# Kernel optimization log

Measured on AMD Instinct MI355X. Metric: run time of the kernel, lower is better.

## Reference

```python
import jax, jax.numpy as jnp
import numpy as np

N_NODES = 500000
FEAT_DIM = 128
BATCH = 50000
K = 16


def setup_inputs() -> dict:
    key = jax.random.key(0)
    k1, k2, k3 = jax.random.split(key, 3)
    features = jax.random.normal(k1, (N_NODES, FEAT_DIM), dtype=jnp.float32)
    # weights = pow(degree, beta); positive floats (uniform in (0.05, 1.05))
    neigh_w = jax.random.uniform(k2, (BATCH, K), dtype=jnp.float32) + 0.05
    neigh_idx = jax.random.randint(k3, (BATCH, K), 0, N_NODES, dtype=jnp.int64)
    return {"features": features, "neigh_w": neigh_w, "neigh_idx": neigh_idx}


def reference(features, neigh_w, neigh_idx):
    # Row-normalize weights (mask = mask.div(mask.sum(1, keepdim=True)))
    w = neigh_w / jnp.sum(neigh_w, axis=-1, keepdims=True)  # [B, K]
    # Gather neighbor embeddings (features(unique_nodes) + sparse mask rows)
    gathered = features[neigh_idx]  # [B, K, D]
    # mask.mm(embed_matrix) == weighted mean over sampled neighbors
    to_feats = jnp.einsum("bk,bkd->bd", w, gathered)  # [B, D]
    return to_feats
```

## Files before the change

### kernel.cpp

```cpp
#include <hip/hip_runtime.h>

#define KNEIGH 16
#define FDIM   128

typedef float f32x4 __attribute__((ext_vector_type(4)));

__global__ __launch_bounds__(256) void WeightedAggregator_89489938580183_kernel(
    const float* __restrict__ features,
    const float* __restrict__ neigh_w,
    const int*   __restrict__ neigh_idx,
    float*       __restrict__ out,
    int batch) {

    const int lane = threadIdx.x & 63;
    int wid = blockIdx.x * (blockDim.x >> 6) + (threadIdx.x >> 6);
    int rowA = wid * 2;
    if (rowA >= batch) return;
    rowA = __builtin_amdgcn_readfirstlane(rowA);
    const int rowB = (rowA + 1 < batch) ? rowA + 1 : rowA;

    const float* wpA = neigh_w   + (size_t)rowA * KNEIGH;
    const float* wpB = neigh_w   + (size_t)rowB * KNEIGH;
    const int*   ipA = neigh_idx + (size_t)rowA * KNEIGH;
    const int*   ipB = neigh_idx + (size_t)rowB * KNEIGH;

    float wA[KNEIGH], wB[KNEIGH];
    int   iA[KNEIGH], iB[KNEIGH];
    #pragma unroll
    for (int k = 0; k < KNEIGH; ++k) {
        wA[k] = wpA[k]; wB[k] = wpB[k];
        iA[k] = ipA[k]; iB[k] = ipB[k];
    }

    float sA = wA[0], sB = wB[0];
    #pragma unroll
    for (int k = 1; k < KNEIGH; ++k) { sA += wA[k]; sB += wB[k]; }
    const float invA = 1.0f / sA;
    const float invB = 1.0f / sB;

    const int half = lane >> 5;
    const int sub  = lane & 31;
    const float inv = half ? invB : invA;

    f32x4 acc0 = (f32x4)(0.0f);
    f32x4 acc1 = (f32x4)(0.0f);

    #pragma unroll
    for (int k = 0; k < KNEIGH; k += 2) {
        const int   i0 = half ? iB[k]     : iA[k];
        const int   i1 = half ? iB[k + 1] : iA[k + 1];
        const float w0 = (half ? wB[k]     : wA[k])     * inv;
        const float w1 = (half ? wB[k + 1] : wA[k + 1]) * inv;

        const f32x4 f0 = ((const f32x4*)features)[((unsigned)i0 << 5) + sub];
        const f32x4 f1 = ((const f32x4*)features)[((unsigned)i1 << 5) + sub];

        acc0 += w0 * f0;
        acc1 += w1 * f1;
    }

    const f32x4 acc = acc0 + acc1;

    const int orow = rowA + half;
    if (orow < batch) {
        f32x4* dst = (f32x4*)(out + (size_t)orow * FDIM) + sub;
        *dst = acc;
    }
}

extern "C" void kernel_launch(void* const* d_in, const int* in_sizes, int n_in,
                              void* d_out, int out_size, void* d_ws, size_t ws_size,
                              hipStream_t stream) {
    const float* features  = (const float*)d_in[0];
    const float* neigh_w   = (const float*)d_in[1];
    const int*   neigh_idx = (const int*)d_in[2];
    float*       out       = (float*)d_out;

    const int batch = in_sizes[1] / KNEIGH;

    const int rows_per_block = 2 * (256 / 64);
    const int blocks = (batch + rows_per_block - 1) / rows_per_block;
    WeightedAggregator_89489938580183_kernel<<<blocks, 256, 0, stream>>>(
        features, neigh_w, neigh_idx, out, batch);
}
```

Before: 351.0 us.

## Partition feature gathers into index slices for cache locality with persistent waves

Launches a fixed grid of waves where each wave handles four row-pairs and makes four passes over the node-index space. On each pass it gathers only the neighbours whose index falls in the current slice of about 131K rows, so all waves work on the same slice of the feature table at roughly the same time. The goal is to shrink the active gather working set to fit in the last-level cache. In exchange, weights and indices are reloaded and the normalisation recomputed on every pass, and waves run with divergent, predicated loads. Nothing synchronises the waves, so they can drift out of step and weaken the locality.

```diff
diff --git a/kernel.cpp b/kernel.cpp
--- a/kernel.cpp
+++ b/kernel.cpp
@@ -2,8 +2,52 @@
 
 #define KNEIGH 16
 #define FDIM   128
+#define NSLICE 4
+#define SLICE_SHIFT 17
+#define NBLOCKS 2048
+#define NWAVES  (NBLOCKS * 4)
 
 typedef float f32x4 __attribute__((ext_vector_type(4)));
+
+__device__ __forceinline__ f32x4 slice_contrib(
+    const float* __restrict__ features,
+    const float* __restrict__ neigh_w,
+    const int*   __restrict__ neigh_idx,
+    int pair, int batch, int half, int sub, unsigned slice) {
+
+    const int r0 = pair * 2;
+    const int r1 = (r0 + 1 < batch) ? r0 + 1 : r0;
+    const float* wp0 = neigh_w   + (size_t)r0 * KNEIGH;
+    const float* wp1 = neigh_w   + (size_t)r1 * KNEIGH;
+    const int*   ip0 = neigh_idx + (size_t)r0 * KNEIGH;
+    const int*   ip1 = neigh_idx + (size_t)r1 * KNEIGH;
+
+    float w0[KNEIGH], w1[KNEIGH]; int i0[KNEIGH], i1[KNEIGH];
+    #pragma unroll
+    for (int k = 0; k < KNEIGH; ++k) {
+        w0[k] = wp0[k]; w1[k] = wp1[k];
+        i0[k] = ip0[k]; i1[k] = ip1[k];
+    }
+    float s0 = w0[0], s1 = w1[0];
+    #pragma unroll
+    for (int k = 1; k < KNEIGH; ++k) { s0 += w0[k]; s1 += w1[k]; }
+    const float inv = half ? (1.0f / s1) : (1.0f / s0);
+
+    f32x4 a0 = (f32x4)(0.0f);
+    f32x4 a1 = (f32x4)(0.0f);
+    #pragma unroll
+    for (int k = 0; k < KNEIGH; k += 2) {
+        const int   iA = half ? i1[k]     : i0[k];
+        const int   iB = half ? i1[k + 1] : i0[k + 1];
+        const float wA = (half ? w1[k]     : w0[k])     * inv;
+        const float wB = (half ? w1[k + 1] : w0[k + 1]) * inv;
+        if (((unsigned)iA >> SLICE_SHIFT) == slice)
+            a0 += wA * ((const f32x4*)features)[((unsigned)iA << 5) + sub];
+        if (((unsigned)iB >> SLICE_SHIFT) == slice)
+            a1 += wB * ((const f32x4*)features)[((unsigned)iB << 5) + sub];
+    }
+    return a0 + a1;
+}
 
 __global__ __launch_bounds__(256) void WeightedAggregator_89489938580183_kernel(
     const float* __restrict__ features,
@@ -13,58 +57,49 @@
     int batch) {
 
     const int lane = threadIdx.x & 63;
-    int wid = blockIdx.x * (blockDim.x >> 6) + (threadIdx.x >> 6);
-    int rowA = wid * 2;
-    if (rowA >= batch) return;
-    rowA = __builtin_amdgcn_readfirstlane(rowA);
-    const int rowB = (rowA + 1 < batch) ? rowA + 1 : rowA;
-
-    const float* wpA = neigh_w   + (size_t)rowA * KNEIGH;
-    const float* wpB = neigh_w   + (size_t)rowB * KNEIGH;
-    const int*   ipA = neigh_idx + (size_t)rowA * KNEIGH;
-    const int*   ipB = neigh_idx + (size_t)rowB * KNEIGH;
-
-    float wA[KNEIGH], wB[KNEIGH];
-    int   iA[KNEIGH], iB[KNEIGH];
-    #pragma unroll
-    for (int k = 0; k < KNEIGH; ++k) {
-        wA[k] = wpA[k]; wB[k] = wpB[k];
-        iA[k] = ipA[k]; iB[k] = ipB[k];
-    }
-
-    float sA = wA[0], sB = wB[0];
-    #pragma unroll
-    for (int k = 1; k < KNEIGH; ++k) { sA += wA[k]; sB += wB[k]; }
-    const float invA = 1.0f / sA;
-    const float invB = 1.0f / sB;
+    const int wid0 = blockIdx.x * (blockDim.x >> 6) + (threadIdx.x >> 6);
+    const int wid  = __builtin_amdgcn_readfirstlane(wid0);
 
     const int half = lane >> 5;
     const int sub  = lane & 31;
-    const float inv = half ? invB : invA;
 
-    f32x4 acc0 = (f32x4)(0.0f);
-    f32x4 acc1 = (f32x4)(0.0f);
+    const int npairs = (batch + 1) >> 1;
+    const int p0 = wid;
+    const int p1 = wid + NWAVES;
+    const int p2 = wid + 2 * NWAVES;
+    const int p3 = wid + 3 * NWAVES;
 
-    #pragma unroll
-    for (int k = 0; k < KNEIGH; k += 2) {
-        const int   i0 = half ? iB[k]     : iA[k];
-        const int   i1 = half ? iB[k + 1] : iA[k + 1];
-        const float w0 = (half ? wB[k]     : wA[k])     * inv;
-        const float w1 = (half ? wB[k + 1] : wA[k + 1]) * inv;
+    f32x4 a0 = (f32x4)(0.0f);
+    f32x4 a1 = (f32x4)(0.0f);
+    f32x4 a2 = (f32x4)(0.0f);
+    f32x4 a3 = (f32x4)(0.0f);
 
-        const f32x4 f0 = ((const f32x4*)features)[((unsigned)i0 << 5) + sub];
-        const f32x4 f1 = ((const f32x4*)features)[((unsigned)i1 << 5) + sub];
-
-        acc0 += w0 * f0;
-        acc1 += w1 * f1;
+    for (unsigned s = 0; s < NSLICE; ++s) {
+        if (p0 < npairs)
+            a0 += slice_contrib(features, neigh_w, neigh_idx, p0, batch, half, sub, s);
+        if (p1 < npairs)
+            a1 += slice_contrib(features, neigh_w, neigh_idx, p1, batch, half, sub, s);
+        if (p2 < npairs)
+            a2 += slice_contrib(features, neigh_w, neigh_idx, p2, batch, half, sub, s);
+        if (p3 < npairs)
+            a3 += slice_contrib(features, neigh_w, neigh_idx, p3, batch, half, sub, s);
     }
 
-    const f32x4 acc = acc0 + acc1;
-
-    const int orow = rowA + half;
-    if (orow < batch) {
-        f32x4* dst = (f32x4*)(out + (size_t)orow * FDIM) + sub;
-        *dst = acc;
+    if (p0 < npairs) {
+        const int orow = p0 * 2 + half;
+        if (orow < batch) ((f32x4*)out)[((size_t)orow << 5) + sub] = a0;
+    }
+    if (p1 < npairs) {
+        const int orow = p1 * 2 + half;
+        if (orow < batch) ((f32x4*)out)[((size_t)orow << 5) + sub] = a1;
+    }
+    if (p2 < npairs) {
+        const int orow = p2 * 2 + half;
+        if (orow < batch) ((f32x4*)out)[((size_t)orow << 5) + sub] = a2;
+    }
+    if (p3 < npairs) {
+        const int orow = p3 * 2 + half;
+        if (orow < batch) ((f32x4*)out)[((size_t)orow << 5) + sub] = a3;
     }
 }
 
@@ -78,8 +113,6 @@
 
     const int batch = in_sizes[1] / KNEIGH;
 
-    const int rows_per_block = 2 * (256 / 64);
-    const int blocks = (batch + rows_per_block - 1) / rows_per_block;
-    WeightedAggregator_89489938580183_kernel<<<blocks, 256, 0, stream>>>(
+    WeightedAggregator_89489938580183_kernel<<<NBLOCKS, 256, 0, stream>>>(
         features, neigh_w, neigh_idx, out, batch);
 }
```

Result: slower. 398.0 us (+13.4%).
